# Performance work log

Hardware: AMD Instinct MI355X
Metric: run time of the kernel (lower is better)

Reference implementation:

```python
import jax, jax.numpy as jnp
import numpy as np

B, N, T, F_IN, H, E = 64, 325, 24, 64, 64, 2600
NEG_SLOPE = 0.2


def setup_inputs() -> dict:
    key = jax.random.key(0)
    k1, k2, k3, k4, k5 = jax.random.split(key, 5)
    x = jax.random.normal(k1, (B, N, T, F_IN), dtype=jnp.float32)
    edge_index = jax.random.randint(k2, (2, E), 0, N, dtype=jnp.int32)
    scale = 1.0 / np.sqrt(F_IN)
    W = jax.random.normal(k3, (H, F_IN), dtype=jnp.float32) * scale
    att_src = jax.random.normal(k4, (H,), dtype=jnp.float32) * scale
    att_dst = jax.random.normal(k5, (H,), dtype=jnp.float32) * scale
    bias = jnp.zeros((H,), dtype=jnp.float32)
    return {"x": x, "edge_index": edge_index, "W": W,
            "att_src": att_src, "att_dst": att_dst, "bias": bias}


def reference(x, edge_index, W, att_src, att_dst, bias):
    b, n, t, nf = x.shape
    # Fold the B*T graph replicas into one leading axis: [G, N, F]
    xg = x.transpose(0, 2, 1, 3).reshape(b * t, n, nf)
    h = jnp.einsum('gnf,hf->gnh', xg, W)  # linear transform [G, N, H]
    a_s = h @ att_src  # [G, N] per-node source attention logit
    a_d = h @ att_dst  # [G, N] per-node dest attention logit
    src, dst = edge_index[0], edge_index[1]
    # Per-edge raw score (gather), LeakyReLU as in GATConv: [G, E]
    e = jax.nn.leaky_relu(a_s[:, src] + a_d[:, dst], negative_slope=NEG_SLOPE)

    def per_graph(e_g, h_g):
        # segment softmax over edges grouped by destination node
        m = jax.ops.segment_max(e_g, dst, num_segments=n)
        ex = jnp.exp(e_g - m[dst])
        den = jax.ops.segment_sum(ex, dst, num_segments=n)
        alpha = ex / den[dst]  # [E]
        msg = alpha[:, None] * h_g[src]  # [E, H]
        return jax.ops.segment_sum(msg, dst, num_segments=n)  # [N, H]

    out = jax.vmap(per_graph)(e, h) + bias  # [G, N, H]
    out = jax.nn.gelu(out, approximate=False)
    # Faithful to source: view(B,T,N,H) then raw reshape(B,N,T,H) (row-major reinterpret)
    return out.reshape(b, n, t, -1)
```

## Files before the change

### kernel.cpp

```cpp
#include <hip/hip_runtime.h>
#include <hip/hip_bf16.h>

#define B_  64
#define N_  325
#define T_  24
#define F_  64
#define H_  64
#define E_  2600
#define G_  (B_ * T_)
#define BLK 512
#define GRID3 512
#define HS  68

using half2_t = __attribute__((ext_vector_type(2))) _Float16;
using half8_t = __attribute__((ext_vector_type(8))) _Float16;
using f32x4   = __attribute__((ext_vector_type(4))) float;

__global__ __launch_bounds__(512) void k_off_prep(
    const int* __restrict__ ei, const float* __restrict__ W,
    const float* __restrict__ att_src, const float* __restrict__ att_dst,
    int* __restrict__ csr_off, unsigned short* __restrict__ perm,
    float* __restrict__ w_sd) {
  __shared__ int cnt[N_];
  const int tid = threadIdx.x;
  for (int i = tid; i < N_; i += BLK) cnt[i] = 0;
  __syncthreads();
  for (int e = tid; e < E_; e += BLK) atomicAdd(&cnt[ei[E_ + e]], 1);
  __syncthreads();
  if (tid <= N_) {
    int off = 0;
    for (int m = 0; m < N_; ++m) off += (m < tid) ? cnt[m] : 0;
    csr_off[tid] = off;
  }
  if (tid < N_) {
    const int c = cnt[tid];
    int r = 0;
    for (int m = 0; m < N_; ++m) {
      const int cm = cnt[m];
      r += (cm > c || (cm == c && m < tid)) ? 1 : 0;
    }
    perm[r] = (unsigned short)tid;
  }
  if (tid < 128) {
    const int k = tid & 63;
    const float* av = (tid < 64) ? att_src : att_dst;
    float s = 0.f;
    for (int h = 0; h < H_; ++h) s += W[h * F_ + k] * av[h];
    w_sd[tid] = s;
  }
}

__global__ __launch_bounds__(64) void k_scatter(const int* __restrict__ ei,
                                                const int* __restrict__ csr_off,
                                                unsigned short* __restrict__ csr_src) {
  __shared__ int dsts[E_];
  const int tid = threadIdx.x;
  for (int i = tid; i < E_; i += 64) dsts[i] = ei[E_ + i];
  __syncthreads();
  const int e = blockIdx.x * 64 + tid;
  if (e >= E_) return;
  const int myd = dsts[e];
  int rank = 0;
#pragma unroll 4
  for (int k = 0; k < e; ++k) rank += (dsts[k] == myd) ? 1 : 0;
  csr_src[csr_off[myd] + rank] = (unsigned short)ei[e];
}

__device__ __forceinline__ float f16lo(unsigned u) {
  half2_t h = __builtin_bit_cast(half2_t, u); return (float)h[0];
}
__device__ __forceinline__ float f16hi(unsigned u) {
  half2_t h = __builtin_bit_cast(half2_t, u); return (float)h[1];
}
__device__ __forceinline__ unsigned short f16b(float f) {
  _Float16 h = (_Float16)f; return __builtin_bit_cast(unsigned short, h);
}
__device__ __forceinline__ half2_t pkrtz(float a, float b) {
  return __builtin_bit_cast(half2_t, __builtin_amdgcn_cvt_pkrtz(a, b));
}
__device__ __forceinline__ half8_t pk8(float4 a, float4 b) {
  half2_t p0 = pkrtz(a.x, a.y);
  half2_t p1 = pkrtz(a.z, a.w);
  half2_t p2 = pkrtz(b.x, b.y);
  half2_t p3 = pkrtz(b.z, b.w);
  half8_t r;
  r[0] = p0[0]; r[1] = p0[1]; r[2] = p1[0]; r[3] = p1[1];
  r[4] = p2[0]; r[5] = p2[1]; r[6] = p3[0]; r[7] = p3[1];
  return r;
}

__device__ __forceinline__ float gelu_f(float v) {
  float t = v * (1.5957691216f + 0.0713550903f * (v * v));
  t = fminf(t, 80.0f);
  float e = __expf(t);
  return v * e * __builtin_amdgcn_rcpf(e + 1.0f);
}

__global__ __launch_bounds__(512, 4) void k_gat3(
    const float* __restrict__ x, const int* __restrict__ csr_off_g,
    const unsigned short* __restrict__ csr_src_g,
    const unsigned short* __restrict__ perm_g, const float* __restrict__ W,
    const float* __restrict__ w_sd, const float* __restrict__ bias,
    float* __restrict__ out) {
  __shared__ _Float16 h_s[N_][HS];
  __shared__ uint2    edge_s[E_];
  __shared__ unsigned asad_s[N_];
  __shared__ float    den_s[N_];
  __shared__ unsigned short coff_s[N_ + 1];
  __shared__ unsigned short perm_s[N_];

  const int tid  = threadIdx.x;
  const int lane = tid & 63;
  const int wv   = tid >> 6;
  const int l15  = lane & 15;
  const int l4   = lane >> 4;

  for (int i = tid; i < E_; i += BLK)
    edge_s[i] = make_uint2(0u, (unsigned)csr_src_g[i]);
  for (int i = tid; i <= N_; i += BLK) coff_s[i] = csr_off_g[i];
  for (int i = tid; i < N_; i += BLK) perm_s[i] = perm_g[i];

  half8_t bf[2][4];
#pragma unroll
  for (int ct = 0; ct < 4; ++ct)
#pragma unroll
    for (int k0 = 0; k0 < 2; ++k0) {
      const float* p = W + (size_t)(ct * 16 + l15) * F_ + k0 * 32 + l4 * 8;
      bf[k0][ct] = pk8(*(const float4*)p, *(const float4*)(p + 4));
    }

  half8_t bw[2];
  {
    const float* wp = w_sd + (l15 & 1) * 64;
#pragma unroll
    for (int k0 = 0; k0 < 2; ++k0) {
      half8_t z = {0, 0, 0, 0, 0, 0, 0, 0};
      const float* p = wp + k0 * 32 + l4 * 8;
      bw[k0] = (l15 < 2) ? pk8(*(const float4*)p, *(const float4*)(p + 4)) : z;
    }
  }

  const int l16v = tid & 15;
  const int qw   = tid >> 4;
  const float4 bias4 = *(const float4*)(bias + 4 * l16v);

  for (int gi = 0; gi < 3; ++gi) {
    const int g  = blockIdx.x + (gi << 9);
    const int bb = g / T_;
    const int tt = g % T_;
    if (gi) __syncthreads();

    const float* xg = x + ((size_t)bb * N_ * T_ + tt) * F_;
    float4 xa[3][4];
#pragma unroll
    for (int ti = 0; ti < 3; ++ti) {
      int t = wv + ti * 8; if (t > 20) t = 20;
      int rr = t * 16 + l15; if (rr > N_ - 1) rr = N_ - 1;
      const float* xr = xg + (size_t)rr * (T_ * F_) + l4 * 8;
      xa[ti][0] = *(const float4*)xr;
      xa[ti][1] = *(const float4*)(xr + 4);
      xa[ti][2] = *(const float4*)(xr + 32);
      xa[ti][3] = *(const float4*)(xr + 36);
    }
#pragma unroll
    for (int ti = 0; ti < 3; ++ti) {
      const int t = wv + ti * 8;
      if (t < 21) {
        const int r0 = t * 16;
        const half8_t a0 = pk8(xa[ti][0], xa[ti][1]);
        const half8_t a1 = pk8(xa[ti][2], xa[ti][3]);
        const bool full = (r0 + 16 <= N_);
#pragma unroll
        for (int ct = 0; ct < 4; ++ct) {
          f32x4 acc = {0.f, 0.f, 0.f, 0.f};
          acc = __builtin_amdgcn_mfma_f32_16x16x32_f16(a0, bf[0][ct], acc, 0, 0, 0);
          acc = __builtin_amdgcn_mfma_f32_16x16x32_f16(a1, bf[1][ct], acc, 0, 0, 0);
          const int col = ct * 16 + l15;
#pragma unroll
          for (int j = 0; j < 4; ++j) {
            const int row = r0 + l4 * 4 + j;
            if (full || row < N_) h_s[row][col] = (_Float16)acc[j];
          }
        }
        f32x4 acc2 = {0.f, 0.f, 0.f, 0.f};
        acc2 = __builtin_amdgcn_mfma_f32_16x16x32_f16(a0, bw[0], acc2, 0, 0, 0);
        acc2 = __builtin_amdgcn_mfma_f32_16x16x32_f16(a1, bw[1], acc2, 0, 0, 0);
        if (l15 < 2) {
#pragma unroll
          for (int j = 0; j < 4; ++j) {
            const int row = r0 + l4 * 4 + j;
            if (full || row < N_)
              ((unsigned short*)asad_s)[row * 2 + l15] = f16b(acc2[j]);
          }
        }
      }
    }
    __syncthreads();

    if (tid < N_) {
      const int n   = perm_s[tid];
      const int beg = coff_s[n], end = coff_s[n + 1];
      const float adn = f16hi(asad_s[n]);
      float den = 0.f;
      for (int p = beg; p < end; ++p) {
        const unsigned sp = edge_s[p].y;
        float e = f16lo(asad_s[sp]) + adn;
        e = fmaxf(e, 0.2f * e);
        const float ex = __expf(e - 5.0f);
        den += ex;
        const unsigned ax = (unsigned)f16b(ex);
        edge_s[p] = make_uint2(ax | (ax << 16), sp);
      }
      den_s[n] = (end > beg) ? (1.0f / den) : 1.0f;
    }
    __syncthreads();

    for (int idx = qw; idx < N_; idx += 32) {
      const int n = perm_s[idx];
      const int beg = coff_s[n], end = coff_s[n + 1];
      half2_t a01 = {(_Float16)0.f, (_Float16)0.f};
      half2_t a23 = {(_Float16)0.f, (_Float16)0.f};
      for (int p = beg; p < end; ++p) {
        const uint2 eu = edge_s[p];
        const half2_t al2 = __builtin_bit_cast(half2_t, eu.x);
        const uint2 hv = *(const uint2*)&h_s[eu.y][4 * l16v];
        a01 = al2 * __builtin_bit_cast(half2_t, hv.x) + a01;
        a23 = al2 * __builtin_bit_cast(half2_t, hv.y) + a23;
      }
      const float inv = den_s[n];
      const float v0 = gelu_f((float)a01[0] * inv + bias4.x);
      const float v1 = gelu_f((float)a01[1] * inv + bias4.y);
      const float v2 = gelu_f((float)a23[0] * inv + bias4.z);
      const float v3 = gelu_f((float)a23[1] * inv + bias4.w);
      *(float4*)&out[((size_t)g * N_ + n) * H_ + 4 * l16v] =
          make_float4(v0, v1, v2, v3);
    }
  }
}

extern "C" void kernel_launch(void* const* d_in, const int* in_sizes, int n_in,
                              void* d_out, int out_size, void* d_ws, size_t ws_size,
                              hipStream_t stream) {
  (void)in_sizes; (void)n_in; (void)out_size; (void)ws_size;
  const float* x       = (const float*)d_in[0];
  const int*   ei      = (const int*)d_in[1];
  const float* W       = (const float*)d_in[2];
  const float* att_src = (const float*)d_in[3];
  const float* att_dst = (const float*)d_in[4];
  const float* bias    = (const float*)d_in[5];
  float* out = (float*)d_out;

  char* ws = (char*)d_ws;
  int*            csr_off = (int*)(ws + 0);
  unsigned short* csr_src = (unsigned short*)(ws + 4096);
  unsigned short* perm    = (unsigned short*)(ws + 16384);
  float*          w_sd    = (float*)(ws + 20480);

  k_off_prep<<<1, BLK, 0, stream>>>(ei, W, att_src, att_dst, csr_off, perm, w_sd);
  k_scatter<<<(E_ + 63) / 64, 64, 0, stream>>>(ei, csr_off, csr_src);
  k_gat3<<<GRID3, BLK, 0, stream>>>(x, csr_off, csr_src, perm, W, w_sd, bias, out);
}
```

Measured before the change: 126.7 us.

## Fuse edge softmax into aggregation and shrink LDS for higher occupancy

Folds the per-destination softmax pass into the aggregation loop, so each 16-lane group computes the edge exponentials itself and accumulates as it goes. This removes the separate denominator phase, one block barrier, the den_s array, and the 8-byte per-edge LDS records, which are replaced by 2-byte source indices. The smaller LDS footprint supports 6 blocks per CU, and the grid grows from 512 to 768 blocks with 2 graphs each instead of 3. In exchange, each of the 16 lanes recomputes the same exp per edge, and exp is now computed with exp2 plus an FMA.

```diff
diff --git a/kernel.cpp b/kernel.cpp
--- a/kernel.cpp
+++ b/kernel.cpp
@@ -9,7 +9,7 @@
 #define E_  2600
 #define G_  (B_ * T_)
 #define BLK 512
-#define GRID3 512
+#define GRID4 768
 #define HS  68
 
 using half2_t = __attribute__((ext_vector_type(2))) _Float16;
@@ -96,16 +96,15 @@
   return v * e * __builtin_amdgcn_rcpf(e + 1.0f);
 }
 
-__global__ __launch_bounds__(512, 4) void k_gat3(
+__global__ __launch_bounds__(512, 6) void k_gat4(
     const float* __restrict__ x, const int* __restrict__ csr_off_g,
     const unsigned short* __restrict__ csr_src_g,
     const unsigned short* __restrict__ perm_g, const float* __restrict__ W,
     const float* __restrict__ w_sd, const float* __restrict__ bias,
     float* __restrict__ out) {
   __shared__ _Float16 h_s[N_][HS];
-  __shared__ uint2    edge_s[E_];
+  __shared__ unsigned short src_s[E_];
   __shared__ unsigned asad_s[N_];
-  __shared__ float    den_s[N_];
   __shared__ unsigned short coff_s[N_ + 1];
   __shared__ unsigned short perm_s[N_];
 
@@ -115,8 +114,7 @@
   const int l15  = lane & 15;
   const int l4   = lane >> 4;
 
-  for (int i = tid; i < E_; i += BLK)
-    edge_s[i] = make_uint2(0u, (unsigned)csr_src_g[i]);
+  for (int i = tid; i < E_; i += BLK) src_s[i] = csr_src_g[i];
   for (int i = tid; i <= N_; i += BLK) coff_s[i] = csr_off_g[i];
   for (int i = tid; i < N_; i += BLK) perm_s[i] = perm_g[i];
 
@@ -144,8 +142,8 @@
   const int qw   = tid >> 4;
   const float4 bias4 = *(const float4*)(bias + 4 * l16v);
 
-  for (int gi = 0; gi < 3; ++gi) {
-    const int g  = blockIdx.x + (gi << 9);
+  for (int gi = 0; gi < 2; ++gi) {
+    const int g  = blockIdx.x + gi * GRID4;
     const int bb = g / T_;
     const int tt = g % T_;
     if (gi) __syncthreads();
@@ -197,37 +195,26 @@
     }
     __syncthreads();
 
-    if (tid < N_) {
-      const int n   = perm_s[tid];
+    for (int idx = qw; idx < N_; idx += 32) {
+      const int n   = perm_s[idx];
       const int beg = coff_s[n], end = coff_s[n + 1];
       const float adn = f16hi(asad_s[n]);
+      half2_t a01 = {(_Float16)0.f, (_Float16)0.f};
+      half2_t a23 = {(_Float16)0.f, (_Float16)0.f};
       float den = 0.f;
       for (int p = beg; p < end; ++p) {
-        const unsigned sp = edge_s[p].y;
-        float e = f16lo(asad_s[sp]) + adn;
+        const int s = src_s[p];
+        float e = f16lo(asad_s[s]) + adn;
         e = fmaxf(e, 0.2f * e);
-        const float ex = __expf(e - 5.0f);
+        const float ex =
+            __builtin_amdgcn_exp2f(__builtin_fmaf(e, 1.44269504f, -7.21347520f));
         den += ex;
-        const unsigned ax = (unsigned)f16b(ex);
-        edge_s[p] = make_uint2(ax | (ax << 16), sp);
-      }
-      den_s[n] = (end > beg) ? (1.0f / den) : 1.0f;
-    }
-    __syncthreads();
-
-    for (int idx = qw; idx < N_; idx += 32) {
-      const int n = perm_s[idx];
-      const int beg = coff_s[n], end = coff_s[n + 1];
-      half2_t a01 = {(_Float16)0.f, (_Float16)0.f};
-      half2_t a23 = {(_Float16)0.f, (_Float16)0.f};
-      for (int p = beg; p < end; ++p) {
-        const uint2 eu = edge_s[p];
-        const half2_t al2 = __builtin_bit_cast(half2_t, eu.x);
-        const uint2 hv = *(const uint2*)&h_s[eu.y][4 * l16v];
+        const half2_t al2 = pkrtz(ex, ex);
+        const uint2 hv = *(const uint2*)&h_s[s][4 * l16v];
         a01 = al2 * __builtin_bit_cast(half2_t, hv.x) + a01;
         a23 = al2 * __builtin_bit_cast(half2_t, hv.y) + a23;
       }
-      const float inv = den_s[n];
+      const float inv = (end > beg) ? __builtin_amdgcn_rcpf(den) : 0.0f;
       const float v0 = gelu_f((float)a01[0] * inv + bias4.x);
       const float v1 = gelu_f((float)a01[1] * inv + bias4.y);
       const float v2 = gelu_f((float)a23[0] * inv + bias4.z);
@@ -258,5 +245,5 @@
 
   k_off_prep<<<1, BLK, 0, stream>>>(ei, W, att_src, att_dst, csr_off, perm, w_sd);
   k_scatter<<<(E_ + 63) / 64, 64, 0, stream>>>(ei, csr_off, csr_src);
-  k_gat3<<<GRID3, BLK, 0, stream>>>(x, csr_off, csr_src, perm, W, w_sd, bias, out);
-}
+  k_gat4<<<GRID4, BLK, 0, stream>>>(x, csr_off, csr_src, perm, W, w_sd, bias, out);
+}
```

Measured after the change: 162.2 us. +28.0%, slower.
